# Kernel optimization log

Measured on AMD Instinct MI355X. Metric: run time of the kernel, lower is better.

Reference implementation:

```python
import jax, jax.numpy as jnp
import numpy as np

EMBED_DIM = 1024
NUM_HEADS = 16
HEAD_DIM = EMBED_DIM // NUM_HEADS
SCALING = HEAD_DIM ** -0.5
T, B = 1024, 4


def setup_inputs() -> dict:
    key = jax.random.key(0)
    k1, k2, k3, k4 = jax.random.split(key, 4)
    x_TBC = jax.random.normal(k1, (T, B, EMBED_DIM), dtype=jnp.float32)
    key_padding_mask = jnp.zeros((B, T), dtype=bool)
    edge_bias = jax.random.normal(k2, (B, NUM_HEADS, T, T), dtype=jnp.float32)
    # xavier_uniform-ish init for weights
    lim_qkv = (6.0 / (EMBED_DIM + 3 * EMBED_DIM)) ** 0.5 / (2 ** 0.5)
    w_qkv = jax.random.uniform(k3, (3 * EMBED_DIM, EMBED_DIM), minval=-lim_qkv, maxval=lim_qkv, dtype=jnp.float32)
    b_qkv = jnp.zeros((3 * EMBED_DIM,), dtype=jnp.float32)
    lim_p = (6.0 / (2 * EMBED_DIM)) ** 0.5
    w_proj = jax.random.uniform(k4, (EMBED_DIM, EMBED_DIM), minval=-lim_p, maxval=lim_p, dtype=jnp.float32)
    b_proj = jnp.zeros((EMBED_DIM,), dtype=jnp.float32)
    return {"x_TBC": x_TBC, "key_padding_mask": key_padding_mask, "edge_bias": edge_bias,
            "w_qkv": w_qkv, "b_qkv": b_qkv, "w_proj": w_proj, "b_proj": b_proj}


def reference(x_TBC, key_padding_mask, edge_bias, w_qkv, b_qkv, w_proj, b_proj):
    Tn, Bn, C = x_TBC.shape
    H, Dh = NUM_HEADS, HEAD_DIM
    qkv = x_TBC @ w_qkv.T + b_qkv               # [T,B,3C]
    q, k, v = jnp.split(qkv, 3, axis=-1)
    def split_heads(t):  # [T,B,C] -> [B,H,T,Dh]
        return t.reshape(Tn, Bn, H, Dh).transpose(1, 2, 0, 3)
    q = split_heads(q) * SCALING
    k = split_heads(k)
    v = split_heads(v)
    logits = jnp.einsum('bhtd,bhsd->bhts', q, k) + edge_bias  # [B,H,T,T]
    neg_inf = jnp.finfo(logits.dtype).min
    logits = jnp.where(key_padding_mask[:, None, None, :], neg_inf, logits)
    attn = jax.nn.softmax(logits, axis=-1)
    out = jnp.einsum('bhts,bhsd->bhtd', attn, v)  # [B,H,T,Dh]
    out = out.transpose(2, 0, 1, 3).reshape(Tn, Bn, C)  # [T,B,C]
    out = out @ w_proj.T + b_proj
    return out
```

## Files before the change

### kernel.cpp

```cpp
#include <hip/hip_runtime.h>
#include <stdint.h>
#include <math.h>

#define TT  1024
#define BBN 4
#define CCH 1024
#define HHN 16
#define DHD 64
#define MMR 4096
#define N3  3072

typedef __attribute__((ext_vector_type(4))) float  f32x4;
typedef __attribute__((ext_vector_type(8))) short  s16x8;
typedef __attribute__((ext_vector_type(8))) __bf16 bf16x8;

static __device__ __forceinline__ f32x4 mfma16(s16x8 a, s16x8 b, f32x4 c) {
  return __builtin_amdgcn_mfma_f32_16x16x32_bf16(
      __builtin_bit_cast(bf16x8, a), __builtin_bit_cast(bf16x8, b), c, 0, 0, 0);
}

static __device__ __forceinline__ unsigned short f2bf(float f) {
  union { float f; unsigned int u; } v; v.f = f;
  unsigned int u = v.u;
  return (unsigned short)((u + 0x7FFFu + ((u >> 16) & 1u)) >> 16);
}

typedef const __attribute__((address_space(1))) void GVoid;
typedef __attribute__((address_space(3))) void LVoid;
static __device__ __forceinline__ void gll16(const void* g, void* l) {
  __builtin_amdgcn_global_load_lds((GVoid*)g, (LVoid*)l, 16, 0, 0);
}

#if __has_builtin(__builtin_amdgcn_exp2f)
#define EXP2F(x) __builtin_amdgcn_exp2f(x)
#else
#define EXP2F(x) exp2f(x)
#endif

__global__ void cvt_all(const float* __restrict__ x, const float* __restrict__ wqkv,
                        const float* __restrict__ wproj, unsigned short* __restrict__ out) {
  int i = blockIdx.x * blockDim.x + threadIdx.x;
  const float4* src;
  int off;
  if (i < 1048576)      { src = (const float4*)x;     off = 0; }
  else if (i < 1835008) { src = (const float4*)wqkv;  off = 1048576; }
  else                  { src = (const float4*)wproj; off = 1835008; }
  float4 f = src[i - off];
  ushort4 o;
  o.x = f2bf(f.x); o.y = f2bf(f.y); o.z = f2bf(f.z); o.w = f2bf(f.w);
  ((ushort4*)out)[i] = o;
}

template <int MODE, int BN>
__global__ __launch_bounds__(256, 3) void gemm_bt(
    const unsigned short* __restrict__ A, const unsigned short* __restrict__ Bw,
    const float* __restrict__ bias, float* __restrict__ Cout,
    unsigned short* __restrict__ qb, unsigned short* __restrict__ kb,
    unsigned short* __restrict__ vtb, int M, int N, int K) {
  constexpr int NI = BN / 32;
  __shared__ __align__(16) unsigned short sMem[128 * 64 + BN * 64];
  unsigned short* sA = sMem;
  unsigned short* sB = sMem + 128 * 64;
  const int tid = threadIdx.x;
  const int l = tid & 63, w = tid >> 6;
  const int g = l >> 4, c = l & 15;
  const int wr = w >> 1, wc = w & 1;
  const int total = gridDim.x * gridDim.y;
  const int flat = blockIdx.y * gridDim.x + blockIdx.x;
  const int wg = (flat & 7) * (total >> 3) + (flat >> 3);
  const int bxs = wg % gridDim.x, bys = wg / gridDim.x;
  const int bm = bys * 128, bn = bxs * BN;
  const int srow = tid >> 3, sch = tid & 7;

  const unsigned short* Agp = A + (size_t)(bm + srow) * K + sch * 8;
  const unsigned short* Bgp = Bw + (size_t)(bn + srow) * K + sch * 8;
  unsigned short* sAw = &sA[w * 512];
  unsigned short* sBw = &sB[w * 512];

  f32x4 acc[4][NI] = {};

  for (int k0 = 0; k0 < K; k0 += 64) {
#pragma unroll
    for (int i = 0; i < 4; ++i)
      gll16(Agp + (size_t)i * 32 * K + k0, sAw + i * 2048);
#pragma unroll
    for (int i = 0; i < BN / 32; ++i)
      gll16(Bgp + (size_t)i * 32 * K + k0, sBw + i * 2048);
    __syncthreads();
#pragma unroll
    for (int kk2 = 0; kk2 < 2; ++kk2) {
      s16x8 af[4], bfr[NI];
#pragma unroll
      for (int mi = 0; mi < 4; ++mi)
        af[mi] = *(const s16x8*)&sA[(wr * 64 + mi * 16 + c) * 64 + kk2 * 32 + g * 8];
#pragma unroll
      for (int ni = 0; ni < NI; ++ni)
        bfr[ni] = *(const s16x8*)&sB[(wc * (BN / 2) + ni * 16 + c) * 64 + kk2 * 32 + g * 8];
#pragma unroll
      for (int mi = 0; mi < 4; ++mi)
#pragma unroll
        for (int ni = 0; ni < NI; ++ni)
          acc[mi][ni] = mfma16(af[mi], bfr[ni], acc[mi][ni]);
    }
    __syncthreads();
  }

  if (MODE == 1 && (bn >> 10) == 2) {
    unsigned short* sT = sMem;
    const int tl0 = bm >> 2;
#pragma unroll
    for (int pc = 0; pc < 2; ++pc) {
      __syncthreads();
      if (wc == pc) {
#pragma unroll
        for (int mi = 0; mi < 4; ++mi)
#pragma unroll
          for (int ni = 0; ni < NI; ++ni) {
            const int col = bn + pc * 64 + ni * 16 + c;
            const float bsv = bias[col];
#pragma unroll
            for (int j = 0; j < 4; ++j)
              sT[(wr * 64 + mi * 16 + g * 4 + j) * 72 + ni * 16 + c] =
                  f2bf(acc[mi][ni][j] + bsv);
          }
      }
      __syncthreads();
      const int h = ((bn + pc * 64) & 1023) >> 6;
      unsigned short* vdst = vtb + ((size_t)(w * 16 + h) * 64 + l) * 1024 + tl0;
#pragma unroll
      for (int q8 = 0; q8 < 4; ++q8) {
        unsigned short pk[8];
#pragma unroll
        for (int e = 0; e < 8; ++e)
          pk[e] = sT[(((q8 * 8 + e) << 2) | w) * 72 + l];
        *(s16x8*)&vdst[q8 * 8] = *(const s16x8*)pk;
      }
    }
    return;
  }

#pragma unroll
  for (int mi = 0; mi < 4; ++mi)
#pragma unroll
    for (int ni = 0; ni < NI; ++ni) {
      const int col = bn + wc * (BN / 2) + ni * 16 + c;
      const float bsv = bias[col];
      if (MODE == 0) {
#pragma unroll
        for (int j = 0; j < 4; ++j) {
          const int r = bm + wr * 64 + mi * 16 + g * 4 + j;
          Cout[(size_t)r * N + col] = acc[mi][ni][j] + bsv;
        }
      } else {
        const int rem = col & 1023;
        const int h = rem >> 6, d = rem & 63;
        const bool isq = (col >> 10) == 0;
        const float qscale = 0.18033688f;
#pragma unroll
        for (int j = 0; j < 4; ++j) {
          const int r = bm + wr * 64 + mi * 16 + g * 4 + j;
          const int t = r >> 2, bb = r & 3;
          const int bh = bb * 16 + h;
          float av = acc[mi][ni][j] + bsv;
          if (isq) qb[((size_t)bh * 1024 + t) * 64 + d] = f2bf(av * qscale);
          else     kb[((size_t)bh * 1024 + t) * 64 + d] = f2bf(av);
        }
      }
    }
}

__global__ __launch_bounds__(256, 3) void attn_kernel(
    const unsigned short* __restrict__ qb, const unsigned short* __restrict__ kb,
    const unsigned short* __restrict__ vtb, const float* __restrict__ eb,
    const unsigned char* __restrict__ mask, unsigned short* __restrict__ ob) {
  __shared__ __align__(16) unsigned short sQ[64 * 64];
  __shared__ __align__(16) unsigned short sK[2][64 * 64];
  __shared__ __align__(16) unsigned short sV[2][64 * 64];
  __shared__ __align__(16) unsigned short sP[4][16 * 72];
  __shared__ __align__(4) unsigned char sM[1024];
  const int tid = threadIdx.x;
  const int l = tid & 63, w = tid >> 6;
  const int g = l >> 4, c = l & 15;
  const int flat = blockIdx.y * 16 + blockIdx.x;
  const int wg = (flat & 7) * 128 + (flat >> 3);
  const int q0 = (wg & 15) * 64;
  const int bh = wg >> 4;
  const int b = bh >> 4;
  const int srow = tid >> 3, sch = tid & 7;

  const unsigned short* qg = qb + (size_t)bh * 65536;
  const unsigned short* kg = kb + (size_t)bh * 65536;
  const unsigned short* vg = vtb + (size_t)bh * 65536;
  const float* ebg = eb + (size_t)bh * 1048576 + (size_t)(q0 + w * 16 + g * 4) * 1024;

  const float BS = 1.44269504f;
  float bvA[4][4], bvB[4][4];
  float ps[4] = {0.f, 0.f, 0.f, 0.f};
  f32x4 po[4] = {};

#define STAGE(tv, P) do {                                                        \
    _Pragma("unroll")                                                            \
    for (int i_ = 0; i_ < 2; ++i_) {                                             \
      int row_ = i_ * 32 + srow;                                                 \
      gll16(kg + (size_t)((tv) * 64 + row_) * 64 + (sch ^ (row_ & 7)) * 8,       \
            &sK[P][i_ * 2048 + w * 512]);                                        \
      gll16(vg + (size_t)row_ * 1024 + (tv) * 64 + (sch ^ (row_ & 7)) * 8,       \
            &sV[P][i_ * 2048 + w * 512]);                                        \
    } } while (0)

#define BIAS(tv, BV) do {                                                        \
    _Pragma("unroll")                                                            \
    for (int ni_ = 0; ni_ < 4; ++ni_)                                            \
      _Pragma("unroll")                                                          \
      for (int j_ = 0; j_ < 4; ++j_)                                             \
        BV[ni_][j_] = ebg[(size_t)j_ * 1024 + (tv) * 64 + ni_ * 16 + c];         \
    } while (0)

#define TILE(P, BV, s0v) do {                                                    \
    float mkc_[4];                                                               \
    _Pragma("unroll")                                                            \
    for (int ni_ = 0; ni_ < 4; ++ni_)                                            \
      mkc_[ni_] = sM[(s0v) + ni_ * 16 + c] ? -1e30f : -8.0f;                     \
    s16x8 kf_[4][2];                                                             \
    _Pragma("unroll")                                                            \
    for (int ni_ = 0; ni_ < 4; ++ni_)                                            \
      _Pragma("unroll")                                                          \
      for (int k2_ = 0; k2_ < 2; ++k2_) {                                        \
        int row_ = ni_ * 16 + c;                                                 \
        kf_[ni_][k2_] = *(const s16x8*)&sK[P][row_ * 64 +                        \
                         (((k2_ * 4 + g) ^ (row_ & 7)) * 8)];                    \
      }                                                                          \
    f32x4 sc_[4] = {};                                                           \
    _Pragma("unroll")                                                            \
    for (int k2_ = 0; k2_ < 2; ++k2_)                                            \
      _Pragma("unroll")                                                          \
      for (int ni_ = 0; ni_ < 4; ++ni_)                                          \
        sc_[ni_] = mfma16(qf[k2_], kf_[ni_][k2_], sc_[ni_]);                     \
    _Pragma("unroll")                                                            \
    for (int ni_ = 0; ni_ < 4; ++ni_)                                            \
      _Pragma("unroll")                                                          \
      for (int j_ = 0; j_ < 4; ++j_) {                                           \
        float x_ = fmaf(BV[ni_][j_], BS, sc_[ni_][j_]) + mkc_[ni_];              \
        float p_ = EXP2F(x_);                                                    \
        sP[w][(g * 4 + j_) * 72 + ni_ * 16 + c] = f2bf(p_);                      \
        ps[j_] += p_;                                                            \
      }                                                                          \
    s16x8 vf_[4][2];                                                             \
    _Pragma("unroll")                                                            \
    for (int nd_ = 0; nd_ < 4; ++nd_)                                            \
      _Pragma("unroll")                                                          \
      for (int k2_ = 0; k2_ < 2; ++k2_) {                                        \
        int row_ = nd_ * 16 + c;                                                 \
        vf_[nd_][k2_] = *(const s16x8*)&sV[P][row_ * 64 +                        \
                         (((k2_ * 4 + g) ^ (row_ & 7)) * 8)];                    \
      }                                                                          \
    asm volatile("s_waitcnt lgkmcnt(0)" ::: "memory");                           \
    __builtin_amdgcn_sched_barrier(0);                                           \
    s16x8 pf_[2];                                                                \
    _Pragma("unroll")                                                            \
    for (int k2_ = 0; k2_ < 2; ++k2_)                                            \
      pf_[k2_] = *(const s16x8*)&sP[w][c * 72 + k2_ * 32 + g * 8];               \
    _Pragma("unroll")                                                            \
    for (int k2_ = 0; k2_ < 2; ++k2_)                                            \
      _Pragma("unroll")                                                          \
      for (int nd_ = 0; nd_ < 4; ++nd_)                                          \
        po[nd_] = mfma16(pf_[k2_], vf_[nd_][k2_], po[nd_]);                      \
  } while (0)

#pragma unroll
  for (int i = 0; i < 2; ++i) {
    int row = i * 32 + srow;
    gll16(qg + (size_t)(q0 + row) * 64 + (sch ^ (row & 7)) * 8, &sQ[i * 2048 + w * 512]);
  }
  STAGE(0, 0);
  STAGE(1, 1);
  BIAS(0, bvA);
  BIAS(1, bvB);
  ((unsigned int*)sM)[tid] = ((const unsigned int*)(mask + b * TT))[tid & 255];
  __syncthreads();

  s16x8 qf[2];
#pragma unroll
  for (int kk2 = 0; kk2 < 2; ++kk2) {
    int row = w * 16 + c;
    qf[kk2] = *(const s16x8*)&sQ[row * 64 + (((kk2 * 4 + g) ^ (row & 7)) * 8)];
  }

#pragma unroll 1
  for (int t2 = 0;; t2 += 2) {
    TILE(0, bvA, t2 * 64);
    __builtin_amdgcn_s_barrier();
    if (t2 + 2 < 16) { STAGE(t2 + 2, 0); BIAS(t2 + 2, bvA); }
    if (t2 == 14) { asm volatile("s_waitcnt vmcnt(16)" ::: "memory"); }
    else          { asm volatile("s_waitcnt vmcnt(36)" ::: "memory"); }
    __builtin_amdgcn_s_barrier();
    TILE(1, bvB, t2 * 64 + 64);
    if (t2 == 14) break;
    __builtin_amdgcn_s_barrier();
    STAGE(t2 + 3, 1); BIAS(t2 + 3, bvB);
    asm volatile("s_waitcnt vmcnt(36)" ::: "memory");
    __builtin_amdgcn_s_barrier();
  }

#undef STAGE
#undef BIAS
#undef TILE

#pragma unroll
  for (int j = 0; j < 4; ++j) {
#pragma unroll
    for (int off = 1; off <= 8; off <<= 1)
      ps[j] += __shfl_xor(ps[j], off, 64);
    ps[j] = 1.0f / ps[j];
  }
  const int h = bh & 15;
#pragma unroll
  for (int nd = 0; nd < 4; ++nd)
#pragma unroll
    for (int j = 0; j < 4; ++j) {
      float val = po[nd][j] * ps[j];
      int t = q0 + w * 16 + g * 4 + j;
      ob[((size_t)t * 4 + b) * 1024 + h * 64 + nd * 16 + c] = f2bf(val);
    }
}

extern "C" void kernel_launch(void* const* d_in, const int* in_sizes, int n_in,
                              void* d_out, int out_size, void* d_ws, size_t ws_size,
                              hipStream_t stream) {
  const float* x      = (const float*)d_in[0];
  const unsigned char* mask = (const unsigned char*)d_in[1];
  const float* ebias  = (const float*)d_in[2];
  const float* wqkv   = (const float*)d_in[3];
  const float* bqkv   = (const float*)d_in[4];
  const float* wproj  = (const float*)d_in[5];
  const float* bproj  = (const float*)d_in[6];
  float* out = (float*)d_out;

  char* ws = (char*)d_ws;
  unsigned short* xb    = (unsigned short*)(ws);
  unsigned short* wqkvb = (unsigned short*)(ws + 8388608);
  unsigned short* wpb   = (unsigned short*)(ws + 14680064);
  unsigned short* qbuf  = (unsigned short*)(ws + 16777216);
  unsigned short* kbuf  = (unsigned short*)(ws + 25165824);
  unsigned short* vtbuf = (unsigned short*)(ws + 33554432);
  unsigned short* obuf  = (unsigned short*)(ws + 41943040);

  cvt_all<<<8192, 256, 0, stream>>>(x, wqkv, wproj, xb);

  gemm_bt<1, 128><<<dim3(24, 32), 256, 0, stream>>>(
      xb, wqkvb, bqkv, nullptr, qbuf, kbuf, vtbuf, MMR, N3, 1024);

  attn_kernel<<<dim3(16, 64), 256, 0, stream>>>(
      qbuf, kbuf, vtbuf, ebias, mask, obuf);

  gemm_bt<0, 64><<<dim3(16, 32), 256, 0, stream>>>(
      obuf, wpb, bproj, out, nullptr, nullptr, nullptr, MMR, 1024, 1024);
}
```

Before: 151.4 us.

## Double-buffer GEMM K-loop with XOR-swizzled LDS and async prefetch

Restructures the bf16 GEMM main loop into a two-stage double buffer over K-slices of 32. The next slice's global-to-LDS loads are issued while the current slice is computed, with explicit vmcnt waits and raw barriers. The LDS layout gets an XOR swizzle to reduce bank conflicts, and the occupancy hint for the MODE 0 GEMM rises to 4 blocks. This aims to hide global load latency and cut LDS conflicts in the QKV and projection GEMMs. The hand-tuned waitcnt counts are fragile and must match the number of loads actually issued.

Measured after the change: 147.4 us. -2.7%, faster.

```diff
diff --git a/kernel.cpp b/kernel.cpp
--- a/kernel.cpp
+++ b/kernel.cpp
@@ -52,15 +52,17 @@
 }
 
 template <int MODE, int BN>
-__global__ __launch_bounds__(256, 3) void gemm_bt(
+__global__ __launch_bounds__(256, MODE == 0 ? 4 : 3) void gemm_bt(
     const unsigned short* __restrict__ A, const unsigned short* __restrict__ Bw,
     const float* __restrict__ bias, float* __restrict__ Cout,
     unsigned short* __restrict__ qb, unsigned short* __restrict__ kb,
     unsigned short* __restrict__ vtb, int M, int N, int K) {
   constexpr int NI = BN / 32;
-  __shared__ __align__(16) unsigned short sMem[128 * 64 + BN * 64];
-  unsigned short* sA = sMem;
-  unsigned short* sB = sMem + 128 * 64;
+  constexpr int AH = 128 * 32;
+  constexpr int BH = BN * 32;
+  __shared__ __align__(16) unsigned short sMem[2 * AH + 2 * BH];
+  unsigned short* sA0 = sMem;
+  unsigned short* sB0 = sMem + 2 * AH;
   const int tid = threadIdx.x;
   const int l = tid & 63, w = tid >> 6;
   const int g = l >> 4, c = l & 15;
@@ -70,40 +72,61 @@
   const int wg = (flat & 7) * (total >> 3) + (flat >> 3);
   const int bxs = wg % gridDim.x, bys = wg / gridDim.x;
   const int bm = bys * 128, bn = bxs * BN;
-  const int srow = tid >> 3, sch = tid & 7;
-
-  const unsigned short* Agp = A + (size_t)(bm + srow) * K + sch * 8;
-  const unsigned short* Bgp = Bw + (size_t)(bn + srow) * K + sch * 8;
-  unsigned short* sAw = &sA[w * 512];
-  unsigned short* sBw = &sB[w * 512];
+
+  const int srow = w * 16 + (l >> 2);
+  const int schG = (l & 3) ^ ((l >> 3) & 3);
+  const unsigned short* Agp = A + (size_t)(bm + srow) * K + schG * 8;
+  const unsigned short* Bgp = Bw + (size_t)(bn + srow) * K + schG * 8;
+  const int swzR = (c >> 1) & 3;
 
   f32x4 acc[4][NI] = {};
 
-  for (int k0 = 0; k0 < K; k0 += 64) {
-#pragma unroll
-    for (int i = 0; i < 4; ++i)
-      gll16(Agp + (size_t)i * 32 * K + k0, sAw + i * 2048);
-#pragma unroll
-    for (int i = 0; i < BN / 32; ++i)
-      gll16(Bgp + (size_t)i * 32 * K + k0, sBw + i * 2048);
-    __syncthreads();
-#pragma unroll
-    for (int kk2 = 0; kk2 < 2; ++kk2) {
-      s16x8 af[4], bfr[NI];
-#pragma unroll
-      for (int mi = 0; mi < 4; ++mi)
-        af[mi] = *(const s16x8*)&sA[(wr * 64 + mi * 16 + c) * 64 + kk2 * 32 + g * 8];
+#define GSTAGE(s, h) do {                                                        \
+    _Pragma("unroll")                                                            \
+    for (int i_ = 0; i_ < 2; ++i_)                                               \
+      gll16(Agp + (size_t)(i_ * 64) * K + (s) * 32,                              \
+            sA0 + (h) * AH + i_ * 2048 + w * 512);                               \
+    _Pragma("unroll")                                                            \
+    for (int i_ = 0; i_ < BN / 64; ++i_)                                         \
+      gll16(Bgp + (size_t)(i_ * 64) * K + (s) * 32,                              \
+            sB0 + (h) * BH + i_ * 2048 + w * 512);                               \
+  } while (0)
+
+#define GWAITN do {                                                              \
+    if constexpr (BN == 128) asm volatile("s_waitcnt vmcnt(4)" ::: "memory");    \
+    else                     asm volatile("s_waitcnt vmcnt(3)" ::: "memory");    \
+  } while (0)
+
+  const int NS = K >> 5;
+  GSTAGE(0, 0);
+  GSTAGE(1, 1);
+  GWAITN;
+  __builtin_amdgcn_s_barrier();
+
+#pragma unroll 1
+  for (int s = 0;; ++s) {
+    const int h = s & 1;
+    s16x8 af[4], bfr[NI];
+#pragma unroll
+    for (int mi = 0; mi < 4; ++mi)
+      af[mi] = *(const s16x8*)&sA0[h * AH + (wr * 64 + mi * 16 + c) * 32 + (g ^ swzR) * 8];
+#pragma unroll
+    for (int ni = 0; ni < NI; ++ni)
+      bfr[ni] = *(const s16x8*)&sB0[h * BH + (wc * (BN / 2) + ni * 16 + c) * 32 + (g ^ swzR) * 8];
+#pragma unroll
+    for (int mi = 0; mi < 4; ++mi)
 #pragma unroll
       for (int ni = 0; ni < NI; ++ni)
-        bfr[ni] = *(const s16x8*)&sB[(wc * (BN / 2) + ni * 16 + c) * 64 + kk2 * 32 + g * 8];
-#pragma unroll
-      for (int mi = 0; mi < 4; ++mi)
-#pragma unroll
-        for (int ni = 0; ni < NI; ++ni)
-          acc[mi][ni] = mfma16(af[mi], bfr[ni], acc[mi][ni]);
-    }
-    __syncthreads();
-  }
+        acc[mi][ni] = mfma16(af[mi], bfr[ni], acc[mi][ni]);
+    if (s == NS - 1) break;
+    __builtin_amdgcn_s_barrier();
+    if (s + 2 < NS) { GSTAGE(s + 2, h); GWAITN; }
+    else            { asm volatile("s_waitcnt vmcnt(0)" ::: "memory"); }
+    __builtin_amdgcn_s_barrier();
+  }
+
+#undef GSTAGE
+#undef GWAITN
 
   if (MODE == 1 && (bn >> 10) == 2) {
     unsigned short* sT = sMem;
@@ -125,8 +148,8 @@
           }
       }
       __syncthreads();
-      const int h = ((bn + pc * 64) & 1023) >> 6;
-      unsigned short* vdst = vtb + ((size_t)(w * 16 + h) * 64 + l) * 1024 + tl0;
+      const int h2 = ((bn + pc * 64) & 1023) >> 6;
+      unsigned short* vdst = vtb + ((size_t)(w * 16 + h2) * 64 + l) * 1024 + tl0;
 #pragma unroll
       for (int q8 = 0; q8 < 4; ++q8) {
         unsigned short pk[8];
```
